# Performance work log

Measured on AMD Instinct MI355X. Metric: run time of the kernel, lower is better.

Reference implementation:

```python
import jax, jax.numpy as jnp
import numpy as np

VOCAB = 185
THRESH = 127.0 / 128.0
S1, S2, S3 = 256, 128, 16
B, L = 262144, 32


def _clamp(x):
    return jnp.clip(x, -THRESH, THRESH)


def setup_inputs() -> dict:
    key = jax.random.key(0)
    ks = jax.random.split(key, 20)
    inp = {
        'pst_idx': jax.random.randint(ks[0], (B, L), 0, 184, dtype=jnp.int64) if jax.config.jax_enable_x64 else jax.random.randint(ks[0], (B, L), 0, 184, dtype=jnp.int32),
        'color_sign': jax.random.normal(ks[1], (B, L), jnp.float32),
        'sob_sign': jax.random.normal(ks[2], (B, L), jnp.float32),
        'wtm': jax.random.uniform(ks[3], (B, 1), jnp.float32),
    }
    isc = 0.72135
    n_symm = 1 + 2 * S1 + 2 * S2
    n_asym = 2 * S1 + S2
    std_s = 1.0 / isc / n_symm ** 0.5
    std_a = 1.0 / isc / n_asym ** 0.5
    std_a2 = 1.0 / isc ** 2 / n_asym ** 0.5
    std_o = 1.0 / isc / (2 * S3) ** 0.5
    std_o2 = 1.0 / isc ** 2 / (2 * S3) ** 0.5
    # embedding tables (divided by 4 as in InputLayer); row 184 is padding (never indexed here)
    inp['emb_fs'] = jax.random.normal(ks[4], (VOCAB, S1), jnp.float32) * 0.25
    inp['emb_va'] = jax.random.normal(ks[5], (VOCAB, S1), jnp.float32) * 0.25
    inp['emb_ha'] = jax.random.normal(ks[6], (VOCAB, S2), jnp.float32) * 0.25
    inp['emb_ra'] = jax.random.normal(ks[7], (VOCAB, S2), jnp.float32) * 0.25
    inp['tempo_w'] = jnp.zeros((S1, 1), jnp.float32)
    # hidden layer weights ([out, in] torch convention)
    inp['fs_w'] = jax.random.normal(ks[8], (S3, S1), jnp.float32) * std_s
    inp['fs_b'] = jax.random.normal(ks[9], (S3,), jnp.float32) * std_s
    inp['absva_w'] = jax.random.normal(ks[10], (S3, S1), jnp.float32) * std_s
    inp['absha_w'] = jax.random.normal(ks[11], (S3, S2), jnp.float32) * std_s
    inp['absra_w'] = jax.random.normal(ks[12], (S3, S2), jnp.float32) * std_s
    inp['va_w'] = jax.random.normal(ks[13], (S3, S1), jnp.float32) * std_a
    inp['fsxva_w'] = jax.random.normal(ks[14], (S3, S1), jnp.float32) * std_a2
    inp['haxra_w'] = jax.random.normal(ks[15], (S3, S2), jnp.float32) * std_a2
    inp['out_va_w'] = jax.random.normal(ks[16], (1, S3), jnp.float32) * std_o
    inp['out_fsxva_w'] = jax.random.normal(ks[17], (1, S3), jnp.float32) * std_o2
    return inp


def _forward(pst_idx, color_sign, sob_sign, wtm, emb_fs, emb_va, emb_ha, emb_ra,
             tempo_w, fs_w, fs_b, absva_w, absha_w, absra_w, va_w, fsxva_w,
             haxra_w, out_va_w, out_fsxva_w):
    b = pst_idx.shape[0]
    rows = jnp.arange(b)[:, None]

    # EmbeddingBag(mode='sum', per_sample_weights=w) == (scatter w into [B,185]) @ table
    def bag(w, table):
        counts = jnp.zeros((b, VOCAB), table.dtype).at[rows, pst_idx].add(w)
        return counts @ table  # [B, s]

    ones = jnp.ones_like(color_sign)
    fs1 = bag(ones, emb_fs)
    va1 = bag(color_sign, emb_va) + wtm @ tempo_w.T
    ha1 = bag(sob_sign, emb_ha)
    ra1 = bag(color_sign * sob_sign, emb_ra)
    fs1, va1, ha1, ra1 = _clamp(fs1), _clamp(va1), _clamp(ha1), _clamp(ra1)

    fs2 = (fs1 @ fs_w.T + fs_b + jnp.abs(va1) @ absva_w.T
           + jnp.abs(ha1) @ absha_w.T + jnp.abs(ra1) @ absra_w.T)
    va2 = va1 @ va_w.T + (fs1 * va1) @ fsxva_w.T + (ha1 * ra1) @ haxra_w.T
    fs2, va2 = _clamp(fs2), _clamp(va2)

    out = va2 @ out_va_w.T + (fs2 * va2) @ out_fsxva_w.T  # [B, 1]
    return jnp.squeeze(out, axis=1)


def reference(pst_idx, color_sign, sob_sign, wtm, emb_fs, emb_va, emb_ha, emb_ra,
              tempo_w, fs_w, fs_b, absva_w, absha_w, absra_w, va_w, fsxva_w,
              haxra_w, out_va_w, out_fsxva_w):
    return _forward(pst_idx, color_sign, sob_sign, wtm, emb_fs, emb_va, emb_ha,
                    emb_ra, tempo_w, fs_w, fs_b, absva_w, absha_w, absra_w,
                    va_w, fsxva_w, haxra_w, out_va_w, out_fsxva_w)
```

## Files before the change

### kernel.cpp

```cpp
#include <hip/hip_runtime.h>
#include <hip/hip_fp16.h>
#include <stdint.h>

typedef _Float16 f16;
typedef _Float16 f16x8 __attribute__((ext_vector_type(8)));
typedef float f32x4 __attribute__((ext_vector_type(4)));

#define NROWS 262144
#define MROWS 16
#define TPB   512
#define GPB   8
#define NBLK  (NROWS / (MROWS * GPB))
#define K     192
#define THR   0.9921875f

#define WS_TABT 0
#define WS_W2FS (768 * 192 * 2)
#define WS_W2VA (WS_W2FS + 16 * 768 * 2)

#define FS_STRIDE 776
#define VA_STRIDE 648
#define VA_BASE   24832
#define EX_BASE   45568
#define PROD_BASE 53760
#define SMEM_SZ   54784

__device__ __forceinline__ f16x8 bc8(uint4 u) {
  union { uint4 u; f16x8 h; } x; x.u = u; return x.h;
}
__device__ __forceinline__ float clampv(float x) {
  return fminf(fmaxf(x, -THR), THR);
}

__global__ void prepack(const float* __restrict__ emb_fs, const float* __restrict__ emb_va,
                        const float* __restrict__ emb_ha, const float* __restrict__ emb_ra,
                        const float* __restrict__ fs_w,   const float* __restrict__ absva_w,
                        const float* __restrict__ absha_w,const float* __restrict__ absra_w,
                        const float* __restrict__ va_w,   const float* __restrict__ fsxva_w,
                        const float* __restrict__ haxra_w, f16* __restrict__ ws) {
  if (blockIdx.x < 24) {
    __shared__ float tile[192 * 33];
    int u0 = blockIdx.x * 32;
    int t = threadIdx.x;
    #pragma unroll 4
    for (int i = 0; i < 24; ++i) {
      int idx = t + 256 * i;
      int k = idx >> 5;
      int c = idx & 31;
      int u = u0 + c;
      float v = 0.f;
      if (k < 185) {
        if      (u < 256) v = emb_fs[k * 256 + u];
        else if (u < 512) v = emb_va[k * 256 + (u - 256)];
        else if (u < 640) v = emb_ha[k * 128 + (u - 512)];
        else              v = emb_ra[k * 128 + (u - 640)];
      }
      tile[k * 33 + c] = v;
    }
    __syncthreads();
    #pragma unroll 4
    for (int i = 0; i < 24; ++i) {
      int idx = t + 256 * i;
      int u = idx / 192;
      int k = idx % 192;
      ws[(u0 + u) * 192 + k] = (f16)tile[k * 33 + u];
    }
  } else {
    int gid = (blockIdx.x - 24) * 256 + threadIdx.x;
    if (gid < 16 * 768) {
      int j = gid / 768, k = gid % 768;
      float v = (k < 256) ? fs_w[j * 256 + k]
              : (k < 512) ? absva_w[j * 256 + (k - 256)]
              : (k < 640) ? absha_w[j * 128 + (k - 512)]
                          : absra_w[j * 128 + (k - 640)];
      ((f16*)((char*)ws + WS_W2FS))[j * 768 + k] = (f16)v;
    } else if (gid < 16 * 768 + 16 * 640) {
      int g = gid - 16 * 768;
      int j = g / 640, k = g % 640;
      float v = (k < 256) ? va_w[j * 256 + k]
              : (k < 512) ? fsxva_w[j * 256 + (k - 256)]
                          : haxra_w[j * 128 + (k - 512)];
      ((f16*)((char*)ws + WS_W2VA))[j * 640 + k] = (f16)v;
    }
  }
}

__global__ __launch_bounds__(TPB, 2)
void rengar_main(const int* __restrict__ pst_idx, const float* __restrict__ color_sign,
                 const float* __restrict__ sob_sign, const float* __restrict__ wtm,
                 const float* __restrict__ tempo_w, const float* __restrict__ fs_b,
                 const float* __restrict__ out_va_w, const float* __restrict__ out_fsxva_w,
                 const f16* __restrict__ ws, float* __restrict__ out) {
  __shared__ __align__(16) char smem[SMEM_SZ];

  const int tid  = threadIdx.x;
  const int lane = tid & 63;
  const int w    = tid >> 6;
  const int l15  = lane & 15;
  const int q    = lane >> 4;

  const f16* tabT = (const f16*)((const char*)ws + WS_TABT);

  uint4 afr1[36];
  int   tbs[6];
  #pragma unroll
  for (int i = 0; i < 6; ++i) {
    int t  = w * 6 + i;
    int u0 = t * 16;
    tbs[i] = (u0 < 256) ? 0 : (u0 < 512) ? 1 : (u0 < 640) ? 2 : 3;
    const f16* ap = tabT + (u0 + l15) * K + q * 8;
    #pragma unroll
    for (int ks = 0; ks < 6; ++ks) afr1[i * 6 + ks] = *(const uint4*)(ap + ks * 32);
  }

  uint4 a2[6];
  if (w < 4) {
    const f16* A = (const f16*)((const char*)ws + WS_W2FS) + l15 * 768 + w * 192 + q * 8;
    #pragma unroll
    for (int ks = 0; ks < 6; ++ks) a2[ks] = *(const uint4*)(A + ks * 32);
  } else {
    const f16* A = (const f16*)((const char*)ws + WS_W2VA) + l15 * 640 + (w - 4) * 160 + q * 8;
    #pragma unroll
    for (int ks = 0; ks < 5; ++ks) a2[ks] = *(const uint4*)(A + ks * 32);
  }

  float bj = 0.f, w1j = 0.f, w2j = 0.f;
  if (tid < 256) {
    int j = tid >> 4;
    bj  = fs_b[j];
    w1j = out_va_w[j];
    w2j = out_fsxva_w[j];
  }

  const int ebase = blockIdx.x * GPB * 512;
  int   vidx = pst_idx[ebase + tid];
  float cc   = color_sign[ebase + tid];
  float ss   = sob_sign[ebase + tid];
  float wtr  = wtm[blockIdx.x * GPB * MROWS + l15];

  #pragma unroll 1
  for (int g = 0; g < GPB; ++g) {
    const int r0 = (blockIdx.x * GPB + g) * MROWS;

    {
      int4 z = make_int4(0, 0, 0, 0);
      int4* p = (int4*)smem;
      #pragma unroll
      for (int i = 0; i < 6; ++i) p[tid + 512 * i] = z;
    }
    __syncthreads();

    {
      int* cntfx = (int*)smem;
      int  row = tid >> 5;
      int* base = cntfx + row * K + vidx;
      atomicAdd(base + 0 * MROWS * K, 65536);
      atomicAdd(base + 1 * MROWS * K, __float2int_rn(cc * 65536.f));
      atomicAdd(base + 2 * MROWS * K, __float2int_rn(ss * 65536.f));
      atomicAdd(base + 3 * MROWS * K, __float2int_rn(cc * ss * 65536.f));
    }
    float nwt = wtr;
    if (g + 1 < GPB) {
      int nb = ebase + (g + 1) * 512;
      vidx = pst_idx[nb + tid];
      cc   = color_sign[nb + tid];
      ss   = sob_sign[nb + tid];
      nwt  = wtm[r0 + MROWS + l15];
    }
    __syncthreads();

    {
      int vals[24];
      const int4* src = (const int4*)smem;
      #pragma unroll
      for (int i = 0; i < 6; ++i) {
        int4 t4 = src[tid * 6 + i];
        vals[4 * i + 0] = t4.x; vals[4 * i + 1] = t4.y;
        vals[4 * i + 2] = t4.z; vals[4 * i + 3] = t4.w;
      }
      __syncthreads();
      int lin = 24 * tid;
      int tb  = lin / 3072;
      int row = (lin / 192) & 15;
      int k0  = lin % 192;
      uint32_t* dst = (uint32_t*)smem + tb * 1600 + row * 100 + (k0 >> 1);
      const float inv = 1.f / 65536.f;
      #pragma unroll
      for (int i = 0; i < 12; ++i) {
        __half2 h = __floats2half2_rn(vals[2 * i] * inv, vals[2 * i + 1] * inv);
        union { __half2 h; uint32_t u; } cv; cv.h = h;
        dst[i] = cv.u;
      }
    }
    __syncthreads();

    f32x4 acc[6];
    {
      uint4 bfr[6];
      int tb_cur = -1;
      #pragma unroll
      for (int i = 0; i < 6; ++i) {
        int tb = tbs[i];
        if (tb != tb_cur) {
          tb_cur = tb;
          #pragma unroll
          for (int ks = 0; ks < 6; ++ks) {
            const uint32_t* p = (const uint32_t*)smem + tb * 1600 + l15 * 100 + ks * 16 + q * 4;
            bfr[ks] = *(const uint4*)p;
          }
        }
        f32x4 a = {0.f, 0.f, 0.f, 0.f};
        #pragma unroll
        for (int ks = 0; ks < 6; ++ks)
          a = __builtin_amdgcn_mfma_f32_16x16x32_f16(bc8(afr1[i * 6 + ks]), bc8(bfr[ks]), a, 0, 0, 0);
        acc[i] = a;
      }
    }
    __syncthreads();

    {
      #pragma unroll
      for (int i = 0; i < 6; ++i) {
        int t  = w * 6 + i;
        int u0 = t * 16;
        int tb = tbs[i];
        int m0 = u0 + q * 4;
        f32x4 a = acc[i];
        if (tb == 0) {
          __half2* d = (__half2*)(smem + l15 * (FS_STRIDE * 2) + m0 * 2);
          d[0] = __floats2half2_rn(clampv(a[0]), clampv(a[1]));
          d[1] = __floats2half2_rn(clampv(a[2]), clampv(a[3]));
        } else if (tb == 1) {
          int s0 = m0 - 256;
          float4 tw = *(const float4*)(tempo_w + s0);
          float b0 = clampv(a[0] + wtr * tw.x);
          float b1 = clampv(a[1] + wtr * tw.y);
          float b2 = clampv(a[2] + wtr * tw.z);
          float b3 = clampv(a[3] + wtr * tw.w);
          __half2* dv = (__half2*)(smem + VA_BASE + l15 * (VA_STRIDE * 2) + s0 * 2);
          dv[0] = __floats2half2_rn(b0, b1);
          dv[1] = __floats2half2_rn(b2, b3);
          __half2* df = (__half2*)(smem + l15 * (FS_STRIDE * 2) + (256 + s0) * 2);
          df[0] = __floats2half2_rn(fabsf(b0), fabsf(b1));
          df[1] = __floats2half2_rn(fabsf(b2), fabsf(b3));
        } else if (tb == 2) {
          int s0 = m0 - 512;
          __half2* d = (__half2*)(smem + l15 * (FS_STRIDE * 2) + (512 + s0) * 2);
          d[0] = __floats2half2_rn(clampv(a[0]), clampv(a[1]));
          d[1] = __floats2half2_rn(clampv(a[2]), clampv(a[3]));
        } else {
          int s0 = m0 - 640;
          __half2* d = (__half2*)(smem + l15 * (FS_STRIDE * 2) + (640 + s0) * 2);
          d[0] = __floats2half2_rn(clampv(a[0]), clampv(a[1]));
          d[1] = __floats2half2_rn(clampv(a[2]), clampv(a[3]));
        }
      }
    }
    __syncthreads();

    {
      uint32_t* fs32 = (uint32_t*)smem;
      uint32_t* va32 = (uint32_t*)(smem + VA_BASE);
      #pragma unroll
      for (int it = 0; it < 6; ++it) {
        int p = tid + 512 * it;
        if (p < 2048) {
          int row = p >> 7, kp = p & 127;
          union { uint32_t u; __half2 h; } a, b, r;
          a.u = fs32[row * 388 + kp];
          b.u = va32[row * 324 + kp];
          r.h = __hmul2(a.h, b.h);
          va32[row * 324 + 128 + kp] = r.u;
        } else {
          int pc = p - 2048;
          int row = pc >> 6, kp = pc & 63;
          union { uint32_t u; __half2 h; } h2, r2, pr;
          h2.u = fs32[row * 388 + 256 + kp];
          r2.u = fs32[row * 388 + 320 + kp];
          pr.h = __hmul2(h2.h, r2.h);
          fs32[row * 388 + 256 + kp] = h2.u & 0x7FFF7FFFu;
          fs32[row * 388 + 320 + kp] = r2.u & 0x7FFF7FFFu;
          va32[row * 324 + 256 + kp] = pr.u;
        }
      }
    }
    __syncthreads();

    float* exch = (float*)(smem + EX_BASE);
    {
      f32x4 a2acc = {0.f, 0.f, 0.f, 0.f};
      if (w < 4) {
        #pragma unroll
        for (int ks = 0; ks < 6; ++ks) {
          int k = w * 192 + ks * 32 + q * 8;
          uint4 bf = *(const uint4*)(smem + l15 * (FS_STRIDE * 2) + k * 2);
          a2acc = __builtin_amdgcn_mfma_f32_16x16x32_f16(bc8(a2[ks]), bc8(bf), a2acc, 0, 0, 0);
        }
      } else {
        #pragma unroll
        for (int ks = 0; ks < 5; ++ks) {
          int k = (w - 4) * 160 + ks * 32 + q * 8;
          uint4 bf = *(const uint4*)(smem + VA_BASE + l15 * (VA_STRIDE * 2) + k * 2);
          a2acc = __builtin_amdgcn_mfma_f32_16x16x32_f16(bc8(a2[ks]), bc8(bf), a2acc, 0, 0, 0);
        }
      }
      #pragma unroll
      for (int r = 0; r < 4; ++r)
        exch[w * 256 + (q * 4 + r) * 16 + l15] = a2acc[r];
    }
    __syncthreads();

    float* prod = (float*)(smem + PROD_BASE);
    if (tid < 256) {
      float f = exch[tid] + exch[256 + tid] + exch[512 + tid] + exch[768 + tid] + bj;
      f = clampv(f);
      float v = exch[1024 + tid] + exch[1280 + tid] + exch[1536 + tid] + exch[1792 + tid];
      v = clampv(v);
      prod[tid] = v * w1j + f * v * w2j;
    }
    __syncthreads();
    if (tid < 16) {
      float s = 0.f;
      #pragma unroll
      for (int j = 0; j < 16; ++j) s += prod[j * 16 + tid];
      out[r0 + tid] = s;
    }
    wtr = nwt;
  }
}

extern "C" void kernel_launch(void* const* d_in, const int* in_sizes, int n_in,
                              void* d_out, int out_size, void* d_ws, size_t ws_size,
                              hipStream_t stream) {
  const int*   pst_idx     = (const int*)  d_in[0];
  const float* color_sign  = (const float*)d_in[1];
  const float* sob_sign    = (const float*)d_in[2];
  const float* wtm         = (const float*)d_in[3];
  const float* emb_fs      = (const float*)d_in[4];
  const float* emb_va      = (const float*)d_in[5];
  const float* emb_ha      = (const float*)d_in[6];
  const float* emb_ra      = (const float*)d_in[7];
  const float* tempo_w     = (const float*)d_in[8];
  const float* fs_b        = (const float*)d_in[10];
  const float* fs_w        = (const float*)d_in[9];
  const float* absva_w     = (const float*)d_in[11];
  const float* absha_w     = (const float*)d_in[12];
  const float* absra_w     = (const float*)d_in[13];
  const float* va_w        = (const float*)d_in[14];
  const float* fsxva_w     = (const float*)d_in[15];
  const float* haxra_w     = (const float*)d_in[16];
  const float* out_va_w    = (const float*)d_in[17];
  const float* out_fsxva_w = (const float*)d_in[18];
  float* out = (float*)d_out;
  f16* ws = (f16*)d_ws;

  prepack<<<24 + 88, 256, 0, stream>>>(emb_fs, emb_va, emb_ha, emb_ra,
                                       fs_w, absva_w, absha_w, absra_w,
                                       va_w, fsxva_w, haxra_w, ws);
  rengar_main<<<NBLK, TPB, 0, stream>>>(pst_idx, color_sign, sob_sign, wtm,
                                        tempo_w, fs_b, out_va_w, out_fsxva_w,
                                        ws, out);
}
```

Baseline: 495.0 us.

## Keep layer-2 inputs wave-local, use float LDS atomics, and cut block barriers

Each wave now owns matching fs/va/ha/ra feature slices, so it can compute the products and abs values in registers and run a partial layer-2 MFMA against per-wave repacked weights. Partial sums from the waves are combined with LDS float atomics. The bag counts are accumulated directly as float atomics and converted to f16 during the fragment load, which removes the fixed-point conversion pass and several __syncthreads. The ha/ra table fragments are reloaded from global memory every group to save registers, and the final output write is deferred by one group with double-buffered exchange space. This adds more atomics and global reloads, and it changes rounding slightly (pkrtz conversion, order-dependent float atomics).

```diff
diff --git a/kernel.cpp b/kernel.cpp
--- a/kernel.cpp
+++ b/kernel.cpp
@@ -11,25 +11,38 @@
 #define TPB   512
 #define GPB   8
 #define NBLK  (NROWS / (MROWS * GPB))
-#define K     192
 #define THR   0.9921875f
 
-#define WS_TABT 0
 #define WS_W2FS (768 * 192 * 2)
-#define WS_W2VA (WS_W2FS + 16 * 768 * 2)
-
-#define FS_STRIDE 776
-#define VA_STRIDE 648
-#define VA_BASE   24832
-#define EX_BASE   45568
-#define PROD_BASE 53760
-#define SMEM_SZ   54784
+#define WS_W2VA (WS_W2FS + 8 * 16 * 96 * 2)
+
+#define CNT_STRIDE 196
+#define TB_FLOATS  (16 * CNT_STRIDE)
+#define EXCH_B 50176
+#define PROW_B 54272
+#define SMEM_SZ 54528
 
 __device__ __forceinline__ f16x8 bc8(uint4 u) {
   union { uint4 u; f16x8 h; } x; x.u = u; return x.h;
 }
 __device__ __forceinline__ float clampv(float x) {
   return fminf(fmaxf(x, -THR), THR);
+}
+__device__ __forceinline__ uint32_t pk2(float a, float b) {
+  union { __half2 h; uint32_t u; } c; c.h = __floats2half2_rn(a, b); return c.u;
+}
+__device__ __forceinline__ uint32_t pkrtz(float a, float b) {
+  union { decltype(__builtin_amdgcn_cvt_pkrtz(0.f, 0.f)) h; uint32_t u; } c;
+  c.h = __builtin_amdgcn_cvt_pkrtz(a, b);
+  return c.u;
+}
+__device__ __forceinline__ uint4 ldfrag(const float* p) {
+  float4 x = *(const float4*)p;
+  float4 y = *(const float4*)(p + 4);
+  uint4 r;
+  r.x = pkrtz(x.x, x.y); r.y = pkrtz(x.z, x.w);
+  r.z = pkrtz(y.x, y.y); r.w = pkrtz(y.z, y.w);
+  return r;
 }
 
 __global__ void prepack(const float* __restrict__ emb_fs, const float* __restrict__ emb_va,
@@ -45,9 +58,7 @@
     #pragma unroll 4
     for (int i = 0; i < 24; ++i) {
       int idx = t + 256 * i;
-      int k = idx >> 5;
-      int c = idx & 31;
-      int u = u0 + c;
+      int k = idx >> 5, c = idx & 31, u = u0 + c;
       float v = 0.f;
       if (k < 185) {
         if      (u < 256) v = emb_fs[k * 256 + u];
@@ -61,26 +72,26 @@
     #pragma unroll 4
     for (int i = 0; i < 24; ++i) {
       int idx = t + 256 * i;
-      int u = idx / 192;
-      int k = idx % 192;
+      int u = idx / 192, k = idx % 192;
       ws[(u0 + u) * 192 + k] = (f16)tile[k * 33 + u];
     }
   } else {
     int gid = (blockIdx.x - 24) * 256 + threadIdx.x;
-    if (gid < 16 * 768) {
-      int j = gid / 768, k = gid % 768;
-      float v = (k < 256) ? fs_w[j * 256 + k]
-              : (k < 512) ? absva_w[j * 256 + (k - 256)]
-              : (k < 640) ? absha_w[j * 128 + (k - 512)]
-                          : absra_w[j * 128 + (k - 640)];
-      ((f16*)((char*)ws + WS_W2FS))[j * 768 + k] = (f16)v;
-    } else if (gid < 16 * 768 + 16 * 640) {
-      int g = gid - 16 * 768;
-      int j = g / 640, k = g % 640;
-      float v = (k < 256) ? va_w[j * 256 + k]
-              : (k < 512) ? fsxva_w[j * 256 + (k - 256)]
-                          : haxra_w[j * 128 + (k - 512)];
-      ((f16*)((char*)ws + WS_W2VA))[j * 640 + k] = (f16)v;
+    if (gid < 12288) {
+      int w = gid / 1536, rem = gid % 1536, j = rem / 96, k = rem % 96;
+      float v = (k < 32) ? fs_w[j * 256 + 32 * w + k]
+              : (k < 64) ? absva_w[j * 256 + 32 * w + (k - 32)]
+              : (k < 80) ? absha_w[j * 128 + 16 * w + (k - 64)]
+                         : absra_w[j * 128 + 16 * w + (k - 80)];
+      ((f16*)((char*)ws + WS_W2FS))[w * 1536 + j * 96 + k] = (f16)v;
+    } else {
+      int g2 = gid - 12288;
+      int w = g2 / 1536, rem = g2 % 1536, j = rem / 96, k = rem % 96;
+      float v = (k < 32) ? va_w[j * 256 + 32 * w + k]
+              : (k < 64) ? fsxva_w[j * 256 + 32 * w + (k - 32)]
+              : (k < 80) ? haxra_w[j * 128 + 16 * w + (k - 64)]
+                         : 0.f;
+      ((f16*)((char*)ws + WS_W2VA))[w * 1536 + j * 96 + k] = (f16)v;
     }
   }
 }
@@ -99,30 +110,34 @@
   const int l15  = lane & 15;
   const int q    = lane >> 4;
 
-  const f16* tabT = (const f16*)((const char*)ws + WS_TABT);
-
-  uint4 afr1[36];
-  int   tbs[6];
-  #pragma unroll
-  for (int i = 0; i < 6; ++i) {
-    int t  = w * 6 + i;
-    int u0 = t * 16;
-    tbs[i] = (u0 < 256) ? 0 : (u0 < 512) ? 1 : (u0 < 640) ? 2 : 3;
-    const f16* ap = tabT + (u0 + l15) * K + q * 8;
+  const f16* tabT = ws;
+
+  uint4 afrA[6], afrB[6], afrC[6], afrD[6];
+  {
+    const f16* pA = tabT + ((size_t)(32 * w + l15)) * 192 + q * 8;
+    const f16* pB = tabT + ((size_t)(32 * w + 16 + l15)) * 192 + q * 8;
+    const f16* pC = tabT + ((size_t)(256 + 32 * w + l15)) * 192 + q * 8;
+    const f16* pD = tabT + ((size_t)(256 + 32 * w + 16 + l15)) * 192 + q * 8;
     #pragma unroll
-    for (int ks = 0; ks < 6; ++ks) afr1[i * 6 + ks] = *(const uint4*)(ap + ks * 32);
-  }
-
-  uint4 a2[6];
-  if (w < 4) {
-    const f16* A = (const f16*)((const char*)ws + WS_W2FS) + l15 * 768 + w * 192 + q * 8;
+    for (int ks = 0; ks < 6; ++ks) {
+      afrA[ks] = *(const uint4*)(pA + ks * 32);
+      afrB[ks] = *(const uint4*)(pB + ks * 32);
+      afrC[ks] = *(const uint4*)(pC + ks * 32);
+      afrD[ks] = *(const uint4*)(pD + ks * 32);
+    }
+  }
+  uint4 a2f[3], a2v[3];
+  {
+    const f16* wf = (const f16*)((const char*)ws + WS_W2FS) + w * 1536 + l15 * 96 + q * 8;
+    const f16* wv = (const f16*)((const char*)ws + WS_W2VA) + w * 1536 + l15 * 96 + q * 8;
     #pragma unroll
-    for (int ks = 0; ks < 6; ++ks) a2[ks] = *(const uint4*)(A + ks * 32);
-  } else {
-    const f16* A = (const f16*)((const char*)ws + WS_W2VA) + l15 * 640 + (w - 4) * 160 + q * 8;
-    #pragma unroll
-    for (int ks = 0; ks < 5; ++ks) a2[ks] = *(const uint4*)(A + ks * 32);
-  }
+    for (int ks = 0; ks < 3; ++ks) {
+      a2f[ks] = *(const uint4*)(wf + ks * 32);
+      a2v[ks] = *(const uint4*)(wv + ks * 32);
+    }
+  }
+  float4 tw0 = *(const float4*)(tempo_w + 32 * w + q * 4);
+  float4 tw1 = *(const float4*)(tempo_w + 32 * w + 16 + q * 4);
 
   float bj = 0.f, w1j = 0.f, w2j = 0.f;
   if (tid < 256) {
@@ -138,26 +153,41 @@
   float ss   = sob_sign[ebase + tid];
   float wtr  = wtm[blockIdx.x * GPB * MROWS + l15];
 
+  char* fb = smem + w * 3328;
+
   #pragma unroll 1
   for (int g = 0; g < GPB; ++g) {
-    const int r0 = (blockIdx.x * GPB + g) * MROWS;
-
-    {
-      int4 z = make_int4(0, 0, 0, 0);
-      int4* p = (int4*)smem;
-      #pragma unroll
-      for (int i = 0; i < 6; ++i) p[tid + 512 * i] = z;
-    }
-    __syncthreads();
-
-    {
-      int* cntfx = (int*)smem;
-      int  row = tid >> 5;
-      int* base = cntfx + row * K + vidx;
-      atomicAdd(base + 0 * MROWS * K, 65536);
-      atomicAdd(base + 1 * MROWS * K, __float2int_rn(cc * 65536.f));
-      atomicAdd(base + 2 * MROWS * K, __float2int_rn(ss * 65536.f));
-      atomicAdd(base + 3 * MROWS * K, __float2int_rn(cc * ss * 65536.f));
+    const int r0  = (blockIdx.x * GPB + g) * MROWS;
+    const int buf = g & 1;
+
+    {
+      uint4 z = make_uint4(0, 0, 0, 0);
+      #pragma unroll
+      for (int it = 0; it < 7; ++it) {
+        int i = tid + 512 * it;
+        if (i < 3264) {
+          char* d = (i < 3136) ? smem + i * 16
+                               : smem + EXCH_B + buf * 2048 + (i - 3136) * 16;
+          *(uint4*)d = z;
+        }
+      }
+    }
+    __syncthreads();
+
+    if (g > 0 && tid < 16) {
+      const float* pr = (const float*)(smem + PROW_B);
+      out[r0 - MROWS + tid] = pr[tid] + pr[16 + tid] + pr[32 + tid] + pr[48 + tid];
+    }
+
+    {
+      float* cnt = (float*)smem;
+      int row = tid >> 5;
+      int idx = row * CNT_STRIDE + vidx;
+      float cs = cc * ss;
+      atomicAdd(cnt + idx + 0 * TB_FLOATS, 1.f);
+      atomicAdd(cnt + idx + 1 * TB_FLOATS, cc);
+      atomicAdd(cnt + idx + 2 * TB_FLOATS, ss);
+      atomicAdd(cnt + idx + 3 * TB_FLOATS, cs);
     }
     float nwt = wtr;
     if (g + 1 < GPB) {
@@ -169,163 +199,115 @@
     }
     __syncthreads();
 
-    {
-      int vals[24];
-      const int4* src = (const int4*)smem;
-      #pragma unroll
-      for (int i = 0; i < 6; ++i) {
-        int4 t4 = src[tid * 6 + i];
-        vals[4 * i + 0] = t4.x; vals[4 * i + 1] = t4.y;
-        vals[4 * i + 2] = t4.z; vals[4 * i + 3] = t4.w;
-      }
-      __syncthreads();
-      int lin = 24 * tid;
-      int tb  = lin / 3072;
-      int row = (lin / 192) & 15;
-      int k0  = lin % 192;
-      uint32_t* dst = (uint32_t*)smem + tb * 1600 + row * 100 + (k0 >> 1);
-      const float inv = 1.f / 65536.f;
-      #pragma unroll
-      for (int i = 0; i < 12; ++i) {
-        __half2 h = __floats2half2_rn(vals[2 * i] * inv, vals[2 * i + 1] * inv);
-        union { __half2 h; uint32_t u; } cv; cv.h = h;
-        dst[i] = cv.u;
-      }
-    }
-    __syncthreads();
-
-    f32x4 acc[6];
-    {
+    f32x4 acc0 = {0,0,0,0}, acc1 = {0,0,0,0}, acc2 = {0,0,0,0},
+          acc3 = {0,0,0,0}, acc4 = {0,0,0,0}, acc5 = {0,0,0,0};
+    {
+      const f16* pE = tabT + ((size_t)(512 + 16 * w + l15)) * 192 + q * 8;
+      const f16* pF = tabT + ((size_t)(640 + 16 * w + l15)) * 192 + q * 8;
+      uint4 afrE[6], afrF[6];
+      #pragma unroll
+      for (int ks = 0; ks < 6; ++ks) {
+        afrE[ks] = *(const uint4*)(pE + ks * 32);
+        afrF[ks] = *(const uint4*)(pF + ks * 32);
+      }
+      const float* cbase = (const float*)smem + l15 * CNT_STRIDE + q * 8;
       uint4 bfr[6];
-      int tb_cur = -1;
-      #pragma unroll
-      for (int i = 0; i < 6; ++i) {
-        int tb = tbs[i];
-        if (tb != tb_cur) {
-          tb_cur = tb;
-          #pragma unroll
-          for (int ks = 0; ks < 6; ++ks) {
-            const uint32_t* p = (const uint32_t*)smem + tb * 1600 + l15 * 100 + ks * 16 + q * 4;
-            bfr[ks] = *(const uint4*)p;
-          }
-        }
-        f32x4 a = {0.f, 0.f, 0.f, 0.f};
-        #pragma unroll
-        for (int ks = 0; ks < 6; ++ks)
-          a = __builtin_amdgcn_mfma_f32_16x16x32_f16(bc8(afr1[i * 6 + ks]), bc8(bfr[ks]), a, 0, 0, 0);
-        acc[i] = a;
-      }
-    }
-    __syncthreads();
-
-    {
-      #pragma unroll
-      for (int i = 0; i < 6; ++i) {
-        int t  = w * 6 + i;
-        int u0 = t * 16;
-        int tb = tbs[i];
-        int m0 = u0 + q * 4;
-        f32x4 a = acc[i];
-        if (tb == 0) {
-          __half2* d = (__half2*)(smem + l15 * (FS_STRIDE * 2) + m0 * 2);
-          d[0] = __floats2half2_rn(clampv(a[0]), clampv(a[1]));
-          d[1] = __floats2half2_rn(clampv(a[2]), clampv(a[3]));
-        } else if (tb == 1) {
-          int s0 = m0 - 256;
-          float4 tw = *(const float4*)(tempo_w + s0);
-          float b0 = clampv(a[0] + wtr * tw.x);
-          float b1 = clampv(a[1] + wtr * tw.y);
-          float b2 = clampv(a[2] + wtr * tw.z);
-          float b3 = clampv(a[3] + wtr * tw.w);
-          __half2* dv = (__half2*)(smem + VA_BASE + l15 * (VA_STRIDE * 2) + s0 * 2);
-          dv[0] = __floats2half2_rn(b0, b1);
-          dv[1] = __floats2half2_rn(b2, b3);
-          __half2* df = (__half2*)(smem + l15 * (FS_STRIDE * 2) + (256 + s0) * 2);
-          df[0] = __floats2half2_rn(fabsf(b0), fabsf(b1));
-          df[1] = __floats2half2_rn(fabsf(b2), fabsf(b3));
-        } else if (tb == 2) {
-          int s0 = m0 - 512;
-          __half2* d = (__half2*)(smem + l15 * (FS_STRIDE * 2) + (512 + s0) * 2);
-          d[0] = __floats2half2_rn(clampv(a[0]), clampv(a[1]));
-          d[1] = __floats2half2_rn(clampv(a[2]), clampv(a[3]));
-        } else {
-          int s0 = m0 - 640;
-          __half2* d = (__half2*)(smem + l15 * (FS_STRIDE * 2) + (640 + s0) * 2);
-          d[0] = __floats2half2_rn(clampv(a[0]), clampv(a[1]));
-          d[1] = __floats2half2_rn(clampv(a[2]), clampv(a[3]));
-        }
-      }
-    }
-    __syncthreads();
-
-    {
-      uint32_t* fs32 = (uint32_t*)smem;
-      uint32_t* va32 = (uint32_t*)(smem + VA_BASE);
-      #pragma unroll
-      for (int it = 0; it < 6; ++it) {
-        int p = tid + 512 * it;
-        if (p < 2048) {
-          int row = p >> 7, kp = p & 127;
-          union { uint32_t u; __half2 h; } a, b, r;
-          a.u = fs32[row * 388 + kp];
-          b.u = va32[row * 324 + kp];
-          r.h = __hmul2(a.h, b.h);
-          va32[row * 324 + 128 + kp] = r.u;
-        } else {
-          int pc = p - 2048;
-          int row = pc >> 6, kp = pc & 63;
-          union { uint32_t u; __half2 h; } h2, r2, pr;
-          h2.u = fs32[row * 388 + 256 + kp];
-          r2.u = fs32[row * 388 + 320 + kp];
-          pr.h = __hmul2(h2.h, r2.h);
-          fs32[row * 388 + 256 + kp] = h2.u & 0x7FFF7FFFu;
-          fs32[row * 388 + 320 + kp] = r2.u & 0x7FFF7FFFu;
-          va32[row * 324 + 256 + kp] = pr.u;
-        }
-      }
-    }
-    __syncthreads();
-
-    float* exch = (float*)(smem + EX_BASE);
-    {
-      f32x4 a2acc = {0.f, 0.f, 0.f, 0.f};
-      if (w < 4) {
-        #pragma unroll
-        for (int ks = 0; ks < 6; ++ks) {
-          int k = w * 192 + ks * 32 + q * 8;
-          uint4 bf = *(const uint4*)(smem + l15 * (FS_STRIDE * 2) + k * 2);
-          a2acc = __builtin_amdgcn_mfma_f32_16x16x32_f16(bc8(a2[ks]), bc8(bf), a2acc, 0, 0, 0);
-        }
-      } else {
-        #pragma unroll
-        for (int ks = 0; ks < 5; ++ks) {
-          int k = (w - 4) * 160 + ks * 32 + q * 8;
-          uint4 bf = *(const uint4*)(smem + VA_BASE + l15 * (VA_STRIDE * 2) + k * 2);
-          a2acc = __builtin_amdgcn_mfma_f32_16x16x32_f16(bc8(a2[ks]), bc8(bf), a2acc, 0, 0, 0);
-        }
-      }
-      #pragma unroll
-      for (int r = 0; r < 4; ++r)
-        exch[w * 256 + (q * 4 + r) * 16 + l15] = a2acc[r];
-    }
-    __syncthreads();
-
-    float* prod = (float*)(smem + PROD_BASE);
+      #pragma unroll
+      for (int ks = 0; ks < 6; ++ks) bfr[ks] = ldfrag(cbase + ks * 32);
+      #pragma unroll
+      for (int ks = 0; ks < 6; ++ks) {
+        acc0 = __builtin_amdgcn_mfma_f32_16x16x32_f16(bc8(afrA[ks]), bc8(bfr[ks]), acc0, 0, 0, 0);
+        acc1 = __builtin_amdgcn_mfma_f32_16x16x32_f16(bc8(afrB[ks]), bc8(bfr[ks]), acc1, 0, 0, 0);
+      }
+      #pragma unroll
+      for (int ks = 0; ks < 6; ++ks) bfr[ks] = ldfrag(cbase + 1 * TB_FLOATS + ks * 32);
+      #pragma unroll
+      for (int ks = 0; ks < 6; ++ks) {
+        acc2 = __builtin_amdgcn_mfma_f32_16x16x32_f16(bc8(afrC[ks]), bc8(bfr[ks]), acc2, 0, 0, 0);
+        acc3 = __builtin_amdgcn_mfma_f32_16x16x32_f16(bc8(afrD[ks]), bc8(bfr[ks]), acc3, 0, 0, 0);
+      }
+      #pragma unroll
+      for (int ks = 0; ks < 6; ++ks) bfr[ks] = ldfrag(cbase + 2 * TB_FLOATS + ks * 32);
+      #pragma unroll
+      for (int ks = 0; ks < 6; ++ks)
+        acc4 = __builtin_amdgcn_mfma_f32_16x16x32_f16(bc8(afrE[ks]), bc8(bfr[ks]), acc4, 0, 0, 0);
+      #pragma unroll
+      for (int ks = 0; ks < 6; ++ks) bfr[ks] = ldfrag(cbase + 3 * TB_FLOATS + ks * 32);
+      #pragma unroll
+      for (int ks = 0; ks < 6; ++ks)
+        acc5 = __builtin_amdgcn_mfma_f32_16x16x32_f16(bc8(afrF[ks]), bc8(bfr[ks]), acc5, 0, 0, 0);
+    }
+    __syncthreads();
+
+    float a0[4], a1[4], b0[4], b1[4], hh[4], rr[4];
+    {
+      float twa[4] = {tw0.x, tw0.y, tw0.z, tw0.w};
+      float twb[4] = {tw1.x, tw1.y, tw1.z, tw1.w};
+      #pragma unroll
+      for (int r = 0; r < 4; ++r) {
+        a0[r] = clampv(acc0[r]);
+        a1[r] = clampv(acc1[r]);
+        b0[r] = clampv(acc2[r] + wtr * twa[r]);
+        b1[r] = clampv(acc3[r] + wtr * twb[r]);
+        hh[r] = clampv(acc4[r]);
+        rr[r] = clampv(acc5[r]);
+      }
+    }
+    const int wrbase = l15 * 208 + q * 8;
+    *(uint2*)(fb + wrbase +   0) = make_uint2(pk2(a0[0], a0[1]), pk2(a0[2], a0[3]));
+    *(uint2*)(fb + wrbase +  32) = make_uint2(pk2(a1[0], a1[1]), pk2(a1[2], a1[3]));
+    *(uint2*)(fb + wrbase +  64) = make_uint2(pk2(fabsf(b0[0]), fabsf(b0[1])), pk2(fabsf(b0[2]), fabsf(b0[3])));
+    *(uint2*)(fb + wrbase +  96) = make_uint2(pk2(fabsf(b1[0]), fabsf(b1[1])), pk2(fabsf(b1[2]), fabsf(b1[3])));
+    *(uint2*)(fb + wrbase + 128) = make_uint2(pk2(fabsf(hh[0]), fabsf(hh[1])), pk2(fabsf(hh[2]), fabsf(hh[3])));
+    *(uint2*)(fb + wrbase + 160) = make_uint2(pk2(fabsf(rr[0]), fabsf(rr[1])), pk2(fabsf(rr[2]), fabsf(rr[3])));
+    f32x4 accf = {0, 0, 0, 0};
+    #pragma unroll
+    for (int ks = 0; ks < 3; ++ks) {
+      uint4 b2 = *(const uint4*)(fb + l15 * 208 + ks * 64 + q * 16);
+      accf = __builtin_amdgcn_mfma_f32_16x16x32_f16(bc8(a2f[ks]), bc8(b2), accf, 0, 0, 0);
+    }
+    *(uint2*)(fb + wrbase +   0) = make_uint2(pk2(b0[0], b0[1]), pk2(b0[2], b0[3]));
+    *(uint2*)(fb + wrbase +  32) = make_uint2(pk2(b1[0], b1[1]), pk2(b1[2], b1[3]));
+    *(uint2*)(fb + wrbase +  64) = make_uint2(pk2(a0[0]*b0[0], a0[1]*b0[1]), pk2(a0[2]*b0[2], a0[3]*b0[3]));
+    *(uint2*)(fb + wrbase +  96) = make_uint2(pk2(a1[0]*b1[0], a1[1]*b1[1]), pk2(a1[2]*b1[2], a1[3]*b1[3]));
+    *(uint2*)(fb + wrbase + 128) = make_uint2(pk2(hh[0]*rr[0], hh[1]*rr[1]), pk2(hh[2]*rr[2], hh[3]*rr[3]));
+    *(uint2*)(fb + wrbase + 160) = make_uint2(0u, 0u);
+    f32x4 accv = {0, 0, 0, 0};
+    #pragma unroll
+    for (int ks = 0; ks < 3; ++ks) {
+      uint4 b2 = *(const uint4*)(fb + l15 * 208 + ks * 64 + q * 16);
+      accv = __builtin_amdgcn_mfma_f32_16x16x32_f16(bc8(a2v[ks]), bc8(b2), accv, 0, 0, 0);
+    }
+
+    {
+      float* ex = (float*)(smem + EXCH_B + buf * 2048);
+      #pragma unroll
+      for (int r = 0; r < 4; ++r) {
+        int idx = (q * 4 + r) * 16 + l15;
+        atomicAdd(ex + idx,       accf[r]);
+        atomicAdd(ex + idx + 256, accv[r]);
+      }
+    }
+    __syncthreads();
+
     if (tid < 256) {
-      float f = exch[tid] + exch[256 + tid] + exch[512 + tid] + exch[768 + tid] + bj;
-      f = clampv(f);
-      float v = exch[1024 + tid] + exch[1280 + tid] + exch[1536 + tid] + exch[1792 + tid];
-      v = clampv(v);
-      prod[tid] = v * w1j + f * v * w2j;
-    }
-    __syncthreads();
-    if (tid < 16) {
-      float s = 0.f;
-      #pragma unroll
-      for (int j = 0; j < 16; ++j) s += prod[j * 16 + tid];
-      out[r0 + tid] = s;
+      const float* ex = (const float*)(smem + EXCH_B + buf * 2048);
+      float f = clampv(ex[tid] + bj);
+      float v = clampv(ex[256 + tid]);
+      float o = v * w1j + f * v * w2j;
+      o += __shfl_xor(o, 16, 64);
+      o += __shfl_xor(o, 32, 64);
+      if (lane < 16)
+        ((float*)(smem + PROW_B))[(tid >> 6) * 16 + lane] = o;
     }
     wtr = nwt;
+  }
+
+  __syncthreads();
+  if (tid < 16) {
+    const float* pr = (const float*)(smem + PROW_B);
+    int r0last = (blockIdx.x * GPB + GPB - 1) * MROWS;
+    out[r0last + tid] = pr[tid] + pr[16 + tid] + pr[32 + tid] + pr[48 + tid];
   }
 }
 
@@ -341,8 +323,8 @@
   const float* emb_ha      = (const float*)d_in[6];
   const float* emb_ra      = (const float*)d_in[7];
   const float* tempo_w     = (const float*)d_in[8];
+  const float* fs_w        = (const float*)d_in[9];
   const float* fs_b        = (const float*)d_in[10];
-  const float* fs_w        = (const float*)d_in[9];
   const float* absva_w     = (const float*)d_in[11];
   const float* absha_w     = (const float*)d_in[12];
   const float* absra_w     = (const float*)d_in[13];
@@ -354,9 +336,9 @@
   float* out = (float*)d_out;
   f16* ws = (f16*)d_ws;
 
-  prepack<<<24 + 88, 256, 0, stream>>>(emb_fs, emb_va, emb_ha, emb_ra,
-                                       fs_w, absva_w, absha_w, absra_w,
-                                       va_w, fsxva_w, haxra_w, ws);
+  prepack<<<120, 256, 0, stream>>>(emb_fs, emb_va, emb_ha, emb_ra,
+                                   fs_w, absva_w, absha_w, absra_w,
+                                   va_w, fsxva_w, haxra_w, ws);
   rengar_main<<<NBLK, TPB, 0, stream>>>(pst_idx, color_sign, sob_sign, wtm,
                                         tempo_w, fs_b, out_va_w, out_fsxva_w,
                                         ws, out);
```

Measured after the change: 884.5 us. +78.7%, slower.
